# Optimization experiments

Measured on AMD Instinct MI355X. Metric: run time of the kernel, lower is better.

The kernel has to match this reference:

```python
import jax, jax.numpy as jnp
import numpy as np

NUM_HEADS = 16
DIM = 1024
B, L = 2, 2048
NEG = -10000000000.0


def setup_inputs() -> dict:
    key = jax.random.key(0)
    ks = jax.random.split(key, 8)
    queries = jax.random.normal(ks[0], (B, L, DIM), dtype=jnp.float32)
    keys = jax.random.normal(ks[1], (B, L, DIM), dtype=jnp.float32)
    values = jax.random.normal(ks[2], (B, L, DIM), dtype=jnp.float32)
    mask = jax.random.uniform(ks[3], (B, L, L)) < 0.1
    s = 1.0 / np.sqrt(DIM)
    Wq = jax.random.uniform(ks[4], (DIM, DIM), minval=-s, maxval=s, dtype=jnp.float32)
    Wk = jax.random.uniform(ks[5], (DIM, DIM), minval=-s, maxval=s, dtype=jnp.float32)
    Wv = jax.random.uniform(ks[6], (DIM, DIM), minval=-s, maxval=s, dtype=jnp.float32)
    Wo = jax.random.uniform(ks[7], (DIM, DIM), minval=-s, maxval=s, dtype=jnp.float32)
    return {"queries": queries, "keys": keys, "values": values, "mask": mask,
            "Wq": Wq, "Wk": Wk, "Wv": Wv, "Wo": Wo}


def reference(queries, keys, values, mask, Wq, Wk, Wv, Wo):
    b, l, d = queries.shape
    h = NUM_HEADS
    dk = d // h
    # torch Linear(bias=False): y = x @ W.T ; then view(b, l, dk, h) -> head axis LAST
    qs = (queries @ Wq.T).reshape(b, l, dk, h)
    ks = (keys @ Wk.T).reshape(b, l, dk, h)
    vs = (values @ Wv.T).reshape(b, l, dk, h)
    # routing is None in the live code path
    w = jnp.einsum('bidh,bodh->bioh', qs, ks) / jnp.sqrt(jnp.asarray(dk, jnp.float32))
    w = jnp.where(mask[..., None], NEG, w)          # masked_fill where mask True
    w = jax.nn.softmax(w, axis=-2)                   # softmax over key axis 'o'
    mha = jnp.einsum('bioh,bodh->bidh', w, vs).reshape(b, l, d)
    # dropout is identity in eval mode
    return mha @ Wo.T
```

## Files before the change

kernel.cpp:

```cpp
#include <hip/hip_runtime.h>
#include <hip/hip_bf16.h>
#include <cstdint>
#include <cstddef>

typedef unsigned short ushort_t;
typedef __attribute__((ext_vector_type(8))) short short8;
typedef __attribute__((ext_vector_type(8))) unsigned short ushort8;
typedef __attribute__((ext_vector_type(4))) unsigned short ushort4v;
typedef __attribute__((ext_vector_type(4))) float f32x4;
typedef __attribute__((ext_vector_type(2))) unsigned long long ull2;
typedef __attribute__((ext_vector_type(2))) unsigned int uint2v;

#define LPAD 72

__device__ __forceinline__ unsigned short f2bf(float f) {
    unsigned int x = __float_as_uint(f);
    unsigned int r = x + 0x7fffu + ((x >> 16) & 1u);
    return (unsigned short)(r >> 16);
}

__device__ __forceinline__ unsigned int cvt_pk_bf16(float lo, float hi) {
    unsigned int r;
    asm("v_cvt_pk_bf16_f32 %0, %1, %2" : "=v"(r) : "v"(lo), "v"(hi));
    return r;
}

__device__ __forceinline__ void async16(const ushort_t* g, ushort_t* l) {
    __builtin_amdgcn_global_load_lds(
        (const __attribute__((address_space(1))) unsigned int*)g,
        (__attribute__((address_space(3))) unsigned int*)l,
        16, 0, 0);
}

__global__ __launch_bounds__(256) void cvt(const float* __restrict__ q,
                                           const float* __restrict__ k,
                                           const float* __restrict__ v,
                                           const float* __restrict__ Wq,
                                           const float* __restrict__ Wk,
                                           const float* __restrict__ Wv,
                                           ushort_t* __restrict__ qb,
                                           ushort_t* __restrict__ kb,
                                           ushort_t* __restrict__ vb,
                                           ushort_t* __restrict__ Wqb,
                                           ushort_t* __restrict__ Wkb,
                                           ushort_t* __restrict__ Wvb) {
    const int z = blockIdx.y;
    const float* X = (z == 0) ? q : (z == 1) ? k : v;
    const float* W = (z == 0) ? Wq : (z == 1) ? Wk : Wv;
    ushort_t* Xo = (z == 0) ? qb : (z == 1) ? kb : vb;
    ushort_t* Wo2 = (z == 0) ? Wqb : (z == 1) ? Wkb : Wvb;
    const size_t idx = (((size_t)blockIdx.x << 8) + threadIdx.x) << 3;
    const float* src; ushort_t* dst; float sc = 1.0f;
    if (idx < 4194304) { src = X + idx; dst = Xo + idx; if (z == 0) sc = 0.125f; }
    else               { src = W + (idx - 4194304); dst = Wo2 + (idx - 4194304); }
    f32x4 a0 = *(const f32x4*)src, a1 = *(const f32x4*)(src + 4);
    ushort8 o;
    #pragma unroll
    for (int j = 0; j < 4; j++) { o[j] = f2bf(a0[j] * sc); o[j + 4] = f2bf(a1[j] * sc); }
    *(ushort8*)dst = o;
}

__global__ __launch_bounds__(256) void maskbits_kernel(const int* __restrict__ mask,
                                                       unsigned long long* __restrict__ Mbits) {
    const int row  = blockIdx.x;
    const int w    = threadIdx.x >> 6;
    const int lane = threadIdx.x & 63;
    const int* mrow = mask + (size_t)row * 2048;
    #pragma unroll
    for (int it = 0; it < 8; it++) {
        const int o = (it << 8) + (w << 6) + lane;
        const unsigned long long bb = __ballot(mrow[o] != 0);
        if (lane == 0) Mbits[(size_t)((it << 2) + w) * 4096 + row] = bb;
    }
}

__global__ __launch_bounds__(256) void woswz(const float* __restrict__ W,
                                             ushort_t* __restrict__ WoH) {
    __shared__ float row[1024 + 64];
    const int j = blockIdx.x, t = threadIdx.x;
    f32x4 v = *(const f32x4*)(W + (size_t)j * 1024 + (t << 2));
    #pragma unroll
    for (int s = 0; s < 4; s++) { const int c = (t << 2) + s; row[c + (c >> 4)] = v[s]; }
    __syncthreads();
    #pragma unroll
    for (int s = 0; s < 4; s++) {
        const int k = t + (s << 8);
        const int col = ((k & 63) << 4) + (k >> 6);
        WoH[(size_t)j * 1024 + k] = f2bf(row[col + (col >> 4)]);
    }
}

__global__ __launch_bounds__(256) void gemm_proj(const ushort_t* __restrict__ qb,
                                                 const ushort_t* __restrict__ kb,
                                                 const ushort_t* __restrict__ vb,
                                                 const ushort_t* __restrict__ Wqb,
                                                 const ushort_t* __restrict__ Wkb,
                                                 const ushort_t* __restrict__ Wvb,
                                                 ushort_t* __restrict__ Qh,
                                                 ushort_t* __restrict__ Kh,
                                                 ushort_t* __restrict__ VhT) {
    __shared__ ushort_t Xs[512 * 8];
    __shared__ ushort_t Ws[512 * 8];

    const int lid  = blockIdx.x;
    const int nIdx = lid / 96;
    const int rem  = lid % 96;
    const int z    = rem >> 5;
    const int mIdx = rem & 31;
    const int n0   = nIdx << 7;
    const int m0   = mIdx << 7;

    const ushort_t* Xb = (z == 0) ? qb : (z == 1) ? kb : vb;
    const ushort_t* Wb = (z == 0) ? Wqb : (z == 1) ? Wkb : Wvb;

    const int tid  = threadIdx.x;
    const int w    = tid >> 6;
    const int lane = tid & 63;
    const int lm   = lane & 15;
    const int quad = lane >> 4;
    const int wm   = w & 1;
    const int wn   = w >> 1;

    f32x4 acc[4][4];
    #pragma unroll
    for (int i = 0; i < 4; i++)
        #pragma unroll
        for (int j = 0; j < 4; j++) acc[i][j] = (f32x4){0.f, 0.f, 0.f, 0.f};

    for (int k0 = 0; k0 < 1024; k0 += 32) {
        __syncthreads();
        #pragma unroll
        for (int i = 0; i < 2; i++) {
            const int L   = (((w << 1) + i) << 6) + lane;
            const int c4  = L >> 7, row = L & 127;
            const int lb  = (((w << 1) + i) << 6) << 3;
            async16(Xb + (size_t)(m0 + row) * 1024 + k0 + (c4 << 3), &Xs[lb]);
            async16(Wb + (size_t)(n0 + row) * 1024 + k0 + (c4 << 3), &Ws[lb]);
        }
        __syncthreads();
        short8 af[4], bf4[4];
        #pragma unroll
        for (int mf = 0; mf < 4; mf++)
            af[mf] = *(const short8*)&Xs[((quad << 7) + (wm << 6) + (mf << 4) + lm) << 3];
        #pragma unroll
        for (int nf = 0; nf < 4; nf++)
            bf4[nf] = *(const short8*)&Ws[((quad << 7) + (wn << 6) + (nf << 4) + lm) << 3];
        #pragma unroll
        for (int mf = 0; mf < 4; mf++)
            #pragma unroll
            for (int nf = 0; nf < 4; nf++)
                acc[mf][nf] = __builtin_amdgcn_mfma_f32_16x16x32_bf16(af[mf], bf4[nf], acc[mf][nf], 0, 0, 0);
    }

    const int bb    = m0 >> 11;
    const int l0    = m0 & 2047;
    const int dbase = (n0 >> 4) + (wn << 2);
    if (z != 2) {
        ushort_t* OUT = (z == 0) ? Qh : Kh;
        #pragma unroll
        for (int mf = 0; mf < 4; mf++)
            #pragma unroll
            for (int r = 0; r < 4; r++) {
                const int row = (wm << 6) + (mf << 4) + (quad << 2) + r;
                ushort4v o = { f2bf(acc[mf][0][r]), f2bf(acc[mf][1][r]),
                               f2bf(acc[mf][2][r]), f2bf(acc[mf][3][r]) };
                *(ushort4v*)(OUT + ((size_t)((bb << 4) + lm) * 2048 + l0 + row) * 64 + dbase) = o;
            }
    } else {
        #pragma unroll
        for (int mf = 0; mf < 4; mf++)
            #pragma unroll
            for (int nf = 0; nf < 4; nf++) {
                const int lbase = l0 + (wm << 6) + (mf << 4) + (quad << 2);
                ushort4v o = { f2bf(acc[mf][nf][0]), f2bf(acc[mf][nf][1]),
                               f2bf(acc[mf][nf][2]), f2bf(acc[mf][nf][3]) };
                *(ushort4v*)(VhT + ((size_t)((bb << 4) + lm) * 64 + dbase + nf) * 2048 + lbase) = o;
            }
    }
}

__global__ __launch_bounds__(256) void gemm_out(const ushort_t* __restrict__ mhaH,
                                                const ushort_t* __restrict__ WoH,
                                                float* __restrict__ C) {
    __shared__ ushort_t Xs[512 * 8];
    __shared__ ushort_t Ws[256 * 8];

    const int lid  = blockIdx.x;
    const int mIdx = ((lid & 7) << 2) | ((lid >> 3) & 3);
    const int nIdx = lid >> 5;
    const int m0   = mIdx << 7;
    const int n0   = nIdx << 6;

    const int tid  = threadIdx.x;
    const int w    = tid >> 6;
    const int lane = tid & 63;
    const int lm   = lane & 15;
    const int quad = lane >> 4;
    const int wm   = w & 1;
    const int wn   = w >> 1;
    const int ab   = m0 >> 11;
    const int al0  = m0 & 2047;

    f32x4 acc[4][2];
    #pragma unroll
    for (int i = 0; i < 4; i++)
        #pragma unroll
        for (int j = 0; j < 2; j++) acc[i][j] = (f32x4){0.f, 0.f, 0.f, 0.f};

    for (int k0 = 0; k0 < 1024; k0 += 32) {
        const int h  = k0 >> 6;
        const int d0 = k0 & 63;
        __syncthreads();
        #pragma unroll
        for (int i = 0; i < 2; i++) {
            const int L   = (i << 8) + (w << 6) + lane;
            const int c4  = L >> 7, row = L & 127;
            async16(mhaH + ((size_t)(ab * 16 + h) * 2048 + al0 + row) * 64 + d0 + (c4 << 3),
                    &Xs[((i << 8) + (w << 6)) << 3]);
        }
        {
            const int L   = (w << 6) + lane;
            const int c4  = L >> 6, row = L & 63;
            async16(WoH + (size_t)(n0 + row) * 1024 + k0 + (c4 << 3),
                    &Ws[(w << 6) << 3]);
        }
        __syncthreads();
        short8 af[4], bf2[2];
        #pragma unroll
        for (int mf = 0; mf < 4; mf++)
            af[mf] = *(const short8*)&Xs[((quad << 7) + (wm << 6) + (mf << 4) + lm) << 3];
        #pragma unroll
        for (int nf = 0; nf < 2; nf++)
            bf2[nf] = *(const short8*)&Ws[((quad << 6) + (wn << 5) + (nf << 4) + lm) << 3];
        #pragma unroll
        for (int mf = 0; mf < 4; mf++)
            #pragma unroll
            for (int nf = 0; nf < 2; nf++)
                acc[mf][nf] = __builtin_amdgcn_mfma_f32_16x16x32_bf16(af[mf], bf2[nf], acc[mf][nf], 0, 0, 0);
    }
    #pragma unroll
    for (int mf = 0; mf < 4; mf++)
        #pragma unroll
        for (int nf = 0; nf < 2; nf++)
            #pragma unroll
            for (int r = 0; r < 4; r++) {
                const int row = m0 + (wm << 6) + (mf << 4) + (quad << 2) + r;
                const int col = n0 + (wn << 5) + (nf << 4) + lm;
                C[(size_t)row * 1024 + col] = acc[mf][nf][r];
            }
}

__global__ __launch_bounds__(256, 2) void flash_attn(const ushort_t* __restrict__ Qh,
                                                     const ushort_t* __restrict__ Kh,
                                                     const ushort_t* __restrict__ VhT,
                                                     const unsigned long long* __restrict__ Mbits,
                                                     ushort_t* __restrict__ mhaH) {
    __shared__ ushort_t Ks[512 * 8];
    __shared__ ushort_t Vs[512 * 8];
    __shared__ ushort_t Pw[4][16 * LPAD];

    const int tid  = threadIdx.x;
    const int w    = tid >> 6;
    const int lane = tid & 63;
    const int lm   = lane & 15;
    const int quad = lane >> 4;
    const int lid  = blockIdx.x;
    const int bh   = ((lid & 7) << 2) | ((lid >> 3) & 3);
    const int q0   = (lid >> 5) << 7;
    const int b    = bh >> 4;

    const ushort_t* Qb  = Qh  + ((size_t)bh << 17);
    const ushort_t* Kb  = Kh  + ((size_t)bh << 17);
    const ushort_t* Vtb = VhT + ((size_t)bh << 17);

    short8 aq[2][2];
    #pragma unroll
    for (int g = 0; g < 2; g++) {
        const ushort_t* qp = Qb + (size_t)(q0 + (w << 5) + (g << 4) + lm) * 64 + (quad << 3);
        aq[g][0] = *(const short8*)qp;
        aq[g][1] = *(const short8*)(qp + 32);
    }

    float l_part[2][4] = {{0.f,0.f,0.f,0.f},{0.f,0.f,0.f,0.f}};
    f32x4 o_acc[2][4] = {{{0.f,0.f,0.f,0.f},{0.f,0.f,0.f,0.f},{0.f,0.f,0.f,0.f},{0.f,0.f,0.f,0.f}},
                         {{0.f,0.f,0.f,0.f},{0.f,0.f,0.f,0.f},{0.f,0.f,0.f,0.f},{0.f,0.f,0.f,0.f}}};

    const int rowbase  = (b << 11) + q0 + (w << 5);
    const int shamt    = (lm & 7) << 2;
    const bool hi_half = lm >= 8;

    const ushort_t* ksrc = Kb  + (size_t)((lm << 2) + w) * 64 + (quad << 3);
    const ushort_t* vsrc = Vtb + (size_t)((w << 4) + lm) * 2048 + (quad << 3);
    ushort_t* kdst0 = &Ks[((w << 7)     ) << 3];
    ushort_t* kdst1 = &Ks[((w << 7) + 64) << 3];
    ushort_t* vdst0 = &Vs[((w << 7)     ) << 3];
    ushort_t* vdst1 = &Vs[((w << 7) + 64) << 3];

    for (int kt0 = 0; kt0 < 2048; kt0 += 64) {
        __syncthreads();
        async16(ksrc + (size_t)kt0 * 64,      kdst0);
        async16(ksrc + (size_t)kt0 * 64 + 32, kdst1);
        async16(vsrc + kt0,      vdst0);
        async16(vsrc + kt0 + 32, vdst1);
        __syncthreads();

        short8 bk[4][2], bv[4][2];
        #pragma unroll
        for (int c = 0; c < 4; c++) {
            bk[c][0] = *(const short8*)&Ks[((c << 7) + lane) << 3];
            bk[c][1] = *(const short8*)&Ks[((c << 7) + 64 + lane) << 3];
            bv[c][0] = *(const short8*)&Vs[((c << 7) + lane) << 3];
            bv[c][1] = *(const short8*)&Vs[((c << 7) + 64 + lane) << 3];
        }

        const unsigned long long* Mt = Mbits + (size_t)(kt0 >> 6) * 4096 + rowbase;

        #pragma unroll
        for (int g = 0; g < 2; g++) {
            f32x4 s[4];
            #pragma unroll
            for (int c = 0; c < 4; c++) {
                f32x4 zz = {0.f, 0.f, 0.f, 0.f};
                zz = __builtin_amdgcn_mfma_f32_16x16x32_bf16(aq[g][0], bk[c][0], zz, 0, 0, 0);
                zz = __builtin_amdgcn_mfma_f32_16x16x32_bf16(aq[g][1], bk[c][1], zz, 0, 0, 0);
                s[c] = zz;
            }
            unsigned long long mb[4];
            {
                const unsigned long long* mp = Mt + (g << 4) + (quad << 2);
                ull2 t0 = *(const ull2*)mp;
                ull2 t1 = *(const ull2*)(mp + 2);
                mb[0] = t0[0]; mb[1] = t0[1]; mb[2] = t1[0]; mb[3] = t1[1];
            }
            #pragma unroll
            for (int r = 0; r < 4; r++) {
                const unsigned long long m64 = mb[r];
                const unsigned word = hi_half ? (unsigned)(m64 >> 32) : (unsigned)m64;
                const unsigned nib  = (word >> shamt) & 0xFu;
                float p0 = __expf(s[0][r]); if (nib & 1u) p0 = 0.f;
                float p1 = __expf(s[1][r]); if (nib & 2u) p1 = 0.f;
                float p2 = __expf(s[2][r]); if (nib & 4u) p2 = 0.f;
                float p3 = __expf(s[3][r]); if (nib & 8u) p3 = 0.f;
                l_part[g][r] += (p0 + p1) + (p2 + p3);
                uint2v pv2;
                pv2[0] = cvt_pk_bf16(p0, p1);
                pv2[1] = cvt_pk_bf16(p2, p3);
                *(uint2v*)&Pw[w][((quad << 2) + r) * LPAD + (lm << 2)] = pv2;
            }
            short8 ap0 = *(const short8*)&Pw[w][lm * LPAD + (quad << 3)];
            short8 ap1 = *(const short8*)&Pw[w][lm * LPAD + 32 + (quad << 3)];
            #pragma unroll
            for (int cd = 0; cd < 4; cd++) {
                o_acc[g][cd] = __builtin_amdgcn_mfma_f32_16x16x32_bf16(ap0, bv[cd][0], o_acc[g][cd], 0, 0, 0);
                o_acc[g][cd] = __builtin_amdgcn_mfma_f32_16x16x32_bf16(ap1, bv[cd][1], o_acc[g][cd], 0, 0, 0);
            }
        }
    }

    #pragma unroll
    for (int g = 0; g < 2; g++) {
        #pragma unroll
        for (int r = 0; r < 4; r++) {
            float l = l_part[g][r];
            l += __shfl_xor(l, 1, 64);
            l += __shfl_xor(l, 2, 64);
            l += __shfl_xor(l, 4, 64);
            l += __shfl_xor(l, 8, 64);
            const float inv_l = 1.0f / l;
            const int i = q0 + (w << 5) + (g << 4) + (quad << 2) + r;
            ushort_t* orow = mhaH + (((size_t)bh * 2048 + i) << 6);
            #pragma unroll
            for (int cd = 0; cd < 4; cd++)
                orow[(cd << 4) + lm] = f2bf(o_acc[g][cd][r] * inv_l);
        }
    }
}

extern "C" void kernel_launch(void* const* d_in, const int* in_sizes, int n_in,
                              void* d_out, int out_size, void* d_ws, size_t ws_size,
                              hipStream_t stream) {
    const float* q    = (const float*)d_in[0];
    const float* k    = (const float*)d_in[1];
    const float* v    = (const float*)d_in[2];
    const int*   mask = (const int*)d_in[3];
    const float* Wq   = (const float*)d_in[4];
    const float* Wk   = (const float*)d_in[5];
    const float* Wv   = (const float*)d_in[6];
    const float* Wo   = (const float*)d_in[7];
    float* out = (float*)d_out;

    ushort_t* qb   = (ushort_t*)d_ws;
    ushort_t* kb   = qb  + 4194304;
    ushort_t* vb   = kb  + 4194304;
    ushort_t* Wqb  = vb  + 4194304;
    ushort_t* Wkb  = Wqb + 1048576;
    ushort_t* Wvb  = Wkb + 1048576;
    ushort_t* Qh   = Wvb + 1048576;
    ushort_t* Kh   = Qh  + 4194304;
    ushort_t* VhT  = Kh  + 4194304;
    ushort_t* mhaH = qb;
    ushort_t* WoH  = kb;
    unsigned long long* Mbits = (unsigned long long*)(kb + 1048576);

    dim3 gb(256);
    cvt<<<dim3(2560, 3), gb, 0, stream>>>(q, k, v, Wq, Wk, Wv, qb, kb, vb, Wqb, Wkb, Wvb);
    gemm_proj<<<dim3(768), gb, 0, stream>>>(qb, kb, vb, Wqb, Wkb, Wvb, Qh, Kh, VhT);
    maskbits_kernel<<<dim3(4096), gb, 0, stream>>>(mask, Mbits);
    woswz<<<dim3(1024), gb, 0, stream>>>(Wo, WoH);
    flash_attn<<<dim3(512), gb, 0, stream>>>(Qh, Kh, VhT, Mbits, mhaH);
    gemm_out<<<dim3(512), gb, 0, stream>>>(mhaH, WoH, out);
}
```

Before: 310.2 us.

## Double-buffer shared-memory tiles in projection, output and attention kernels

Converts the single-buffered LDS staging in the QKV projection GEMM, the output GEMM and the attention kernel into ping-pong double buffers. The next tile's async global-to-LDS copy is issued before computing on the current tile, and one barrier per iteration replaces two. This is meant to hide global load latency behind MFMA work, at the cost of doubled LDS use, which may lower occupancy. Correctness depends on async16 completion being covered by the barrier before the buffers swap.

```diff
diff --git a/kernel.cpp b/kernel.cpp
--- a/kernel.cpp
+++ b/kernel.cpp
@@ -99,8 +99,8 @@
                                                  ushort_t* __restrict__ Qh,
                                                  ushort_t* __restrict__ Kh,
                                                  ushort_t* __restrict__ VhT) {
-    __shared__ ushort_t Xs[512 * 8];
-    __shared__ ushort_t Ws[512 * 8];
+    __shared__ ushort_t Xs[2][4096];
+    __shared__ ushort_t Ws[2][4096];
 
     const int lid  = blockIdx.x;
     const int nIdx = lid / 96;
@@ -127,29 +127,36 @@
         #pragma unroll
         for (int j = 0; j < 4; j++) acc[i][j] = (f32x4){0.f, 0.f, 0.f, 0.f};
 
-    for (int k0 = 0; k0 < 1024; k0 += 32) {
-        __syncthreads();
+    auto stage = [&](int k0, int buf) {
         #pragma unroll
         for (int i = 0; i < 2; i++) {
             const int L   = (((w << 1) + i) << 6) + lane;
             const int c4  = L >> 7, row = L & 127;
             const int lb  = (((w << 1) + i) << 6) << 3;
-            async16(Xb + (size_t)(m0 + row) * 1024 + k0 + (c4 << 3), &Xs[lb]);
-            async16(Wb + (size_t)(n0 + row) * 1024 + k0 + (c4 << 3), &Ws[lb]);
-        }
-        __syncthreads();
+            async16(Xb + (size_t)(m0 + row) * 1024 + k0 + (c4 << 3), &Xs[buf][lb]);
+            async16(Wb + (size_t)(n0 + row) * 1024 + k0 + (c4 << 3), &Ws[buf][lb]);
+        }
+    };
+
+    stage(0, 0);
+    __syncthreads();
+
+    int cur = 0;
+    for (int t = 0; t < 32; ++t) {
+        if (t < 31) stage((t + 1) << 5, cur ^ 1);
         short8 af[4], bf4[4];
         #pragma unroll
         for (int mf = 0; mf < 4; mf++)
-            af[mf] = *(const short8*)&Xs[((quad << 7) + (wm << 6) + (mf << 4) + lm) << 3];
+            af[mf] = *(const short8*)&Xs[cur][((quad << 7) + (wm << 6) + (mf << 4) + lm) << 3];
         #pragma unroll
         for (int nf = 0; nf < 4; nf++)
-            bf4[nf] = *(const short8*)&Ws[((quad << 7) + (wn << 6) + (nf << 4) + lm) << 3];
+            bf4[nf] = *(const short8*)&Ws[cur][((quad << 7) + (wn << 6) + (nf << 4) + lm) << 3];
         #pragma unroll
         for (int mf = 0; mf < 4; mf++)
             #pragma unroll
             for (int nf = 0; nf < 4; nf++)
                 acc[mf][nf] = __builtin_amdgcn_mfma_f32_16x16x32_bf16(af[mf], bf4[nf], acc[mf][nf], 0, 0, 0);
+        if (t < 31) { __syncthreads(); cur ^= 1; }
     }
 
     const int bb    = m0 >> 11;
@@ -182,8 +189,8 @@
 __global__ __launch_bounds__(256) void gemm_out(const ushort_t* __restrict__ mhaH,
                                                 const ushort_t* __restrict__ WoH,
                                                 float* __restrict__ C) {
-    __shared__ ushort_t Xs[512 * 8];
-    __shared__ ushort_t Ws[256 * 8];
+    __shared__ ushort_t Xs[2][4096];
+    __shared__ ushort_t Ws[2][2048];
 
     const int lid  = blockIdx.x;
     const int mIdx = ((lid & 7) << 2) | ((lid >> 3) & 3);
@@ -207,36 +214,43 @@
         #pragma unroll
         for (int j = 0; j < 2; j++) acc[i][j] = (f32x4){0.f, 0.f, 0.f, 0.f};
 
-    for (int k0 = 0; k0 < 1024; k0 += 32) {
+    auto stage = [&](int k0, int buf) {
         const int h  = k0 >> 6;
         const int d0 = k0 & 63;
-        __syncthreads();
         #pragma unroll
         for (int i = 0; i < 2; i++) {
             const int L   = (i << 8) + (w << 6) + lane;
             const int c4  = L >> 7, row = L & 127;
             async16(mhaH + ((size_t)(ab * 16 + h) * 2048 + al0 + row) * 64 + d0 + (c4 << 3),
-                    &Xs[((i << 8) + (w << 6)) << 3]);
+                    &Xs[buf][((i << 8) + (w << 6)) << 3]);
         }
         {
             const int L   = (w << 6) + lane;
             const int c4  = L >> 6, row = L & 63;
             async16(WoH + (size_t)(n0 + row) * 1024 + k0 + (c4 << 3),
-                    &Ws[(w << 6) << 3]);
-        }
-        __syncthreads();
+                    &Ws[buf][(w << 6) << 3]);
+        }
+    };
+
+    stage(0, 0);
+    __syncthreads();
+
+    int cur = 0;
+    for (int t = 0; t < 32; ++t) {
+        if (t < 31) stage((t + 1) << 5, cur ^ 1);
         short8 af[4], bf2[2];
         #pragma unroll
         for (int mf = 0; mf < 4; mf++)
-            af[mf] = *(const short8*)&Xs[((quad << 7) + (wm << 6) + (mf << 4) + lm) << 3];
+            af[mf] = *(const short8*)&Xs[cur][((quad << 7) + (wm << 6) + (mf << 4) + lm) << 3];
         #pragma unroll
         for (int nf = 0; nf < 2; nf++)
-            bf2[nf] = *(const short8*)&Ws[((quad << 6) + (wn << 5) + (nf << 4) + lm) << 3];
+            bf2[nf] = *(const short8*)&Ws[cur][((quad << 6) + (wn << 5) + (nf << 4) + lm) << 3];
         #pragma unroll
         for (int mf = 0; mf < 4; mf++)
             #pragma unroll
             for (int nf = 0; nf < 2; nf++)
                 acc[mf][nf] = __builtin_amdgcn_mfma_f32_16x16x32_bf16(af[mf], bf2[nf], acc[mf][nf], 0, 0, 0);
+        if (t < 31) { __syncthreads(); cur ^= 1; }
     }
     #pragma unroll
     for (int mf = 0; mf < 4; mf++)
@@ -255,8 +269,8 @@
                                                      const ushort_t* __restrict__ VhT,
                                                      const unsigned long long* __restrict__ Mbits,
                                                      ushort_t* __restrict__ mhaH) {
-    __shared__ ushort_t Ks[512 * 8];
-    __shared__ ushort_t Vs[512 * 8];
+    __shared__ ushort_t Ks[2][4096];
+    __shared__ ushort_t Vs[2][4096];
     __shared__ ushort_t Pw[4][16 * LPAD];
 
     const int tid  = threadIdx.x;
@@ -291,26 +305,29 @@
 
     const ushort_t* ksrc = Kb  + (size_t)((lm << 2) + w) * 64 + (quad << 3);
     const ushort_t* vsrc = Vtb + (size_t)((w << 4) + lm) * 2048 + (quad << 3);
-    ushort_t* kdst0 = &Ks[((w << 7)     ) << 3];
-    ushort_t* kdst1 = &Ks[((w << 7) + 64) << 3];
-    ushort_t* vdst0 = &Vs[((w << 7)     ) << 3];
-    ushort_t* vdst1 = &Vs[((w << 7) + 64) << 3];
-
-    for (int kt0 = 0; kt0 < 2048; kt0 += 64) {
-        __syncthreads();
-        async16(ksrc + (size_t)kt0 * 64,      kdst0);
-        async16(ksrc + (size_t)kt0 * 64 + 32, kdst1);
-        async16(vsrc + kt0,      vdst0);
-        async16(vsrc + kt0 + 32, vdst1);
-        __syncthreads();
+
+    auto stageKV = [&](int kt0, int buf) {
+        async16(ksrc + (size_t)kt0 * 64,      &Ks[buf][((w << 7)     ) << 3]);
+        async16(ksrc + (size_t)kt0 * 64 + 32, &Ks[buf][((w << 7) + 64) << 3]);
+        async16(vsrc + kt0,      &Vs[buf][((w << 7)     ) << 3]);
+        async16(vsrc + kt0 + 32, &Vs[buf][((w << 7) + 64) << 3]);
+    };
+
+    stageKV(0, 0);
+    __syncthreads();
+
+    int cur = 0;
+    for (int t = 0; t < 32; ++t) {
+        const int kt0 = t << 6;
+        if (t < 31) stageKV(kt0 + 64, cur ^ 1);
 
         short8 bk[4][2], bv[4][2];
         #pragma unroll
         for (int c = 0; c < 4; c++) {
-            bk[c][0] = *(const short8*)&Ks[((c << 7) + lane) << 3];
-            bk[c][1] = *(const short8*)&Ks[((c << 7) + 64 + lane) << 3];
-            bv[c][0] = *(const short8*)&Vs[((c << 7) + lane) << 3];
-            bv[c][1] = *(const short8*)&Vs[((c << 7) + 64 + lane) << 3];
+            bk[c][0] = *(const short8*)&Ks[cur][((c << 7) + lane) << 3];
+            bk[c][1] = *(const short8*)&Ks[cur][((c << 7) + 64 + lane) << 3];
+            bv[c][0] = *(const short8*)&Vs[cur][((c << 7) + lane) << 3];
+            bv[c][1] = *(const short8*)&Vs[cur][((c << 7) + 64 + lane) << 3];
         }
 
         const unsigned long long* Mt = Mbits + (size_t)(kt0 >> 6) * 4096 + rowbase;
@@ -355,6 +372,7 @@
                 o_acc[g][cd] = __builtin_amdgcn_mfma_f32_16x16x32_bf16(ap1, bv[cd][1], o_acc[g][cd], 0, 0, 0);
             }
         }
+        if (t < 31) { __syncthreads(); cur ^= 1; }
     }
 
     #pragma unroll
```

New measurement: 324.1 us. 1.04x slower.
